# Performance work log

Measured on AMD Instinct MI355X. Metric: run time of the kernel, lower is better.

The kernel has to match this reference:

```python
import math
import jax, jax.numpy as jnp
import numpy as np

CANTOR_DEPTH = 8
CANTOR_TEMPERATURE = 1.0
SEQ_LEN = 4096


def _cantor_positions(depth_max):
    positions = [np.array([0.0, 1.0])]
    for _ in range(1, depth_max):
        prev = positions[-1]
        new = []
        for i in range(len(prev) - 1):
            left = prev[i]
            right = prev[i + 1]
            third = (right - left) / 3.0
            new.append(left)
            new.append(left + third)
        new.append(prev[-1])
        positions.append(np.array(new))
    return positions


def _cantor_indices(seq_len, depth_max):
    # indices[d] = unique sorted long indices of Cantor positions at depth d
    pos = _cantor_positions(depth_max)
    out = []
    for d in range(depth_max):
        idx = np.unique((pos[d] * (seq_len - 1)).astype(np.int64))
        out.append(jnp.asarray(idx))
    return out


# number of depths actually used in the forward loop
_N_DEPTHS = min(CANTOR_DEPTH, int(math.log2(SEQ_LEN)) + 2)
# get_cantor_indices caps depth at cantor_depth - 1 implicitly via list length
CANTOR_IDX = _cantor_indices(SEQ_LEN, CANTOR_DEPTH)


def setup_inputs() -> dict:
    key0 = jax.random.key(0)
    ks = jax.random.split(key0, 4)
    B, S, D = 8, SEQ_LEN, 512
    return {
        "query": jax.random.normal(ks[0], (B, S, D), dtype=jnp.float32),
        "key": jax.random.normal(ks[1], (B, S, D), dtype=jnp.float32),
        "value": jax.random.normal(ks[2], (B, S, D), dtype=jnp.float32),
        "t": jax.random.normal(ks[3], (B,), dtype=jnp.float32),
        "scale_weights": jnp.ones((CANTOR_DEPTH,), dtype=jnp.float32),
        "scale_temperature": jnp.ones((1,), dtype=jnp.float32),
    }


def reference(query, key, value, t, scale_weights, scale_temperature):
    D = key.shape[-1]
    inv_scale = 1.0 / (math.sqrt(D) * CANTOR_TEMPERATURE)
    scale_outputs = []
    for depth in range(_N_DEPTHS):
        idx = CANTOR_IDX[depth]            # static, <= 2^depth + 1 indices
        sk = key[:, idx]                   # [B, Nd, D] gather
        sv = value[:, idx]                 # [B, Nd, D]
        scores = jnp.einsum("bqd,bkd->bqk", query, sk) * inv_scale
        attn = jax.nn.softmax(scores, axis=-1)
        scale_outputs.append(jnp.einsum("bqk,bkd->bqd", attn, sv))
    stacked = jnp.stack(scale_outputs, axis=0)  # [depths, B, Q, D]
    w = jax.nn.softmax(scale_weights[: len(scale_outputs)] / scale_temperature[0])
    out = jnp.sum(stacked * w[:, None, None, None], axis=0)  # [B, Q, D]
    # torch .squeeze(1) is a no-op here since Q != 1
    return out
```

## Files before the change

### kernel.cpp

```cpp
#include <hip/hip_runtime.h>

#define NDEPTH 8
#define NK 129
#define SEQB 4096
#define DIM 512

typedef short bf16x8 __attribute__((ext_vector_type(8)));
typedef float f32x4  __attribute__((ext_vector_type(4)));

struct CTab { int uidx[NK]; int minD[NK]; int count; };

static constexpr CTab make_ctab() {
    CTab T{};
    double pos[NDEPTH][NK] = {}; int cnt[NDEPTH] = {};
    pos[0][0] = 0.0; pos[0][1] = 1.0; cnt[0] = 2;
    for (int d = 1; d < NDEPTH; ++d) {
        const int n = cnt[d - 1]; int m = 0;
        for (int i = 0; i < n - 1; ++i) {
            const double left = pos[d - 1][i], right = pos[d - 1][i + 1];
            const double third = (right - left) / 3.0;
            pos[d][m++] = left; pos[d][m++] = left + third;
        }
        pos[d][m++] = pos[d - 1][n - 1]; cnt[d] = m;
    }
    int idx[NDEPTH][NK] = {}; int icnt[NDEPTH] = {};
    for (int d = 0; d < NDEPTH; ++d) {
        int m = 0;
        for (int i = 0; i < cnt[d]; ++i) {
            const long long v = (long long)(pos[d][i] * 4095.0);
            bool dup = false;
            for (int k = 0; k < m; ++k) if (idx[d][k] == (int)v) dup = true;
            if (!dup) idx[d][m++] = (int)v;
        }
        icnt[d] = m;
    }
    int u[2 * NK] = {}; int un = 0;
    for (int d = 0; d < NDEPTH; ++d)
        for (int i = 0; i < icnt[d]; ++i) {
            const int v = idx[d][i]; bool f = false;
            for (int k = 0; k < un; ++k) if (u[k] == v) f = true;
            if (!f && un < 2 * NK) u[un++] = v;
        }
    for (int i = 1; i < un; ++i) {
        const int key = u[i]; int k = i - 1;
        while (k >= 0 && u[k] > key) { u[k + 1] = u[k]; --k; }
        u[k + 1] = key;
    }
    T.count = un;
    for (int i = 0; i < un && i < NK; ++i) {
        T.uidx[i] = u[i];
        int md = NDEPTH;
        for (int d = 0; d < NDEPTH && md == NDEPTH; ++d)
            for (int k = 0; k < icnt[d]; ++k)
                if (idx[d][k] == u[i]) { md = d; break; }
        T.minD[i] = md;
    }
    return T;
}
static constexpr CTab h_ct = make_ctab();
static_assert(h_ct.count == NK, "cantor union size mismatch");
__device__ __constant__ CTab g_ct = h_ct;

__device__ __forceinline__ short f2bf(float f) {
    union { float f; unsigned u; } v; v.f = f;
    unsigned r = v.u + 0x7fffu + ((v.u >> 16) & 1u);
    return (short)(r >> 16);
}

#define WSK_ELEMS (8 * 144 * 512)

__global__ __launch_bounds__(256) void ufa_prep(
    const float* __restrict__ K, const float* __restrict__ V,
    short* __restrict__ ws)
{
    short* wsK  = ws;
    short* wsVt = ws + WSK_ELEMS;
    if (blockIdx.x < 1152) {
        const int b = blockIdx.x / 144, key = blockIdx.x % 144;
        short* dst = wsK + ((size_t)b * 144 + key) * 512;
        if (key < NK) {
            const float* src = K + ((size_t)b * SEQB + g_ct.uidx[key]) * DIM;
            for (int i = threadIdx.x; i < 512; i += 256) dst[i] = f2bf(src[i]);
        } else {
            for (int i = threadIdx.x; i < 512; i += 256) dst[i] = 0;
        }
    } else {
        __shared__ float tr[16][132];
        const int id = blockIdx.x - 1152;
        const int b = id >> 5, dc = id & 31;
        const float* Vb = V + (size_t)b * SEQB * DIM + dc * 16;
        const int kk = (int)threadIdx.x >> 4, d = (int)threadIdx.x & 15;
        #pragma unroll
        for (int it = 0; it < 9; ++it) {
            const int k = it * 16 + kk;
            if (k < NK) tr[d][k] = Vb[(size_t)g_ct.uidx[k] * DIM + d];
        }
        __syncthreads();
        short* dst = wsVt + ((size_t)b * 512 + dc * 16) * 192;
        for (int idx = threadIdx.x; idx < 16 * 192; idx += 256) {
            const int dd = idx / 192, k = idx - dd * 192;
            dst[idx] = (k < NK) ? f2bf(tr[dd][k]) : (short)0;
        }
    }
}

__global__ __launch_bounds__(64, 4) void ufa_main(
    const float* __restrict__ Q, const short* __restrict__ ws,
    const float* __restrict__ SW, const float* __restrict__ ST,
    float* __restrict__ Out)
{
    __shared__ short c_lds[16 * 200];

    const short* wsK  = ws;
    const short* wsVt = ws + WSK_ELEMS;

    const int lane = (int)threadIdx.x;
    const int m    = lane & 15;
    const int quad = lane >> 4;
    const int b    = (int)blockIdx.x >> 8;
    const int q0   = ((int)blockIdx.x & 255) << 4;

    float wgt[NDEPTH];
    {
        const float it = 1.0f / ST[0];
        float mx = -3.0e38f;
        #pragma unroll
        for (int d = 0; d < NDEPTH; ++d) { wgt[d] = SW[d] * it; mx = fmaxf(mx, wgt[d]); }
        float sum = 0.0f;
        #pragma unroll
        for (int d = 0; d < NDEPTH; ++d) { wgt[d] = __expf(wgt[d] - mx); sum += wgt[d]; }
        const float is = 1.0f / sum;
        #pragma unroll
        for (int d = 0; d < NDEPTH; ++d) wgt[d] *= is;
    }

    f32x4 acc[9];
    #pragma unroll
    for (int tt = 0; tt < 9; ++tt) acc[tt] = (f32x4){0.f, 0.f, 0.f, 0.f};

    const float* Qb = Q + ((size_t)b * SEQB + q0 + m) * DIM;
    const short* Kb = wsK + (size_t)b * 144 * 512;

    #pragma unroll
    for (int c = 0; c < 8; ++c) {
        bf16x8 aq[2];
        #pragma unroll
        for (int ks = 0; ks < 2; ++ks) {
            const float* qp = Qb + c * 64 + ks * 32 + quad * 8;
            const float4 x = *(const float4*)qp;
            const float4 y = *(const float4*)(qp + 4);
            aq[ks][0] = f2bf(x.x); aq[ks][1] = f2bf(x.y);
            aq[ks][2] = f2bf(x.z); aq[ks][3] = f2bf(x.w);
            aq[ks][4] = f2bf(y.x); aq[ks][5] = f2bf(y.y);
            aq[ks][6] = f2bf(y.z); aq[ks][7] = f2bf(y.w);
        }
        #pragma unroll
        for (int ks = 0; ks < 2; ++ks) {
            #pragma unroll
            for (int tt = 0; tt < 9; ++tt) {
                const bf16x8 bk = *(const bf16x8*)&Kb[(size_t)(tt * 16 + m) * 512
                                                     + c * 64 + ks * 32 + quad * 8];
                acc[tt] = __builtin_amdgcn_mfma_f32_16x16x32_bf16(aq[ks], bk, acc[tt], 0, 0, 0);
            }
        }
    }

    const float inv_scale = 0.04419417382415922f;
    int md9[9];
    #pragma unroll
    for (int tt = 0; tt < 9; ++tt) {
        const int j = tt * 16 + m;
        md9[tt] = (j < NK) ? g_ct.minD[j] : NDEPTH;
    }
    float ev[9][4], mxr[4];
    #pragma unroll
    for (int i = 0; i < 4; ++i) mxr[i] = -3.0e38f;
    #pragma unroll
    for (int tt = 0; tt < 9; ++tt) {
        const bool valid = (tt * 16 + m) < NK;
        #pragma unroll
        for (int i = 0; i < 4; ++i) {
            const float s = valid ? acc[tt][i] * inv_scale : -3.0e38f;
            ev[tt][i] = s;
            mxr[i] = fmaxf(mxr[i], s);
        }
    }
    #pragma unroll
    for (int off = 1; off < 16; off <<= 1)
        #pragma unroll
        for (int i = 0; i < 4; ++i) mxr[i] = fmaxf(mxr[i], __shfl_xor(mxr[i], off));

    float P[4][NDEPTH];
    #pragma unroll
    for (int i = 0; i < 4; ++i)
        #pragma unroll
        for (int d = 0; d < NDEPTH; ++d) P[i][d] = 0.0f;
    #pragma unroll
    for (int tt = 0; tt < 9; ++tt) {
        const int md = md9[tt];
        #pragma unroll
        for (int i = 0; i < 4; ++i) {
            const float e = __expf(ev[tt][i] - mxr[i]);
            ev[tt][i] = e;
            #pragma unroll
            for (int d = 0; d < NDEPTH; ++d) P[i][d] += (md == d) ? e : 0.0f;
        }
    }
    #pragma unroll
    for (int off = 1; off < 16; off <<= 1)
        #pragma unroll
        for (int i = 0; i < 4; ++i)
            #pragma unroll
            for (int d = 0; d < NDEPTH; ++d) P[i][d] += __shfl_xor(P[i][d], off);

    float T[4][NDEPTH];
    #pragma unroll
    for (int i = 0; i < 4; ++i) {
        float L = 0.0f, Lc[NDEPTH];
        #pragma unroll
        for (int d = 0; d < NDEPTH; ++d) { L += P[i][d]; Lc[d] = L; }
        float ta = 0.0f;
        #pragma unroll
        for (int d = NDEPTH - 1; d >= 0; --d) { ta += wgt[d] / Lc[d]; T[i][d] = ta; }
    }
    #pragma unroll
    for (int tt = 0; tt < 10; ++tt) {
        const int j = tt * 16 + m;
        #pragma unroll
        for (int i = 0; i < 4; ++i) {
            float cv = 0.0f;
            if (tt < 9 && j < NK) {
                const int md = md9[tt];
                float tv = 0.0f;
                #pragma unroll
                for (int d = 0; d < NDEPTH; ++d) tv = (md == d) ? T[i][d] : tv;
                cv = ev[tt][i] * tv;
            }
            c_lds[(quad * 4 + i) * 200 + j] = f2bf(cv);
        }
    }
    __syncthreads();

    bf16x8 ac[5];
    #pragma unroll
    for (int ks = 0; ks < 5; ++ks)
        ac[ks] = *(const bf16x8*)&c_lds[m * 200 + ks * 32 + quad * 8];

    const short* Vtb = wsVt + (size_t)b * 512 * 192;
    float* Ob = Out + ((size_t)b * SEQB + q0) * DIM;

    #pragma unroll
    for (int c2 = 0; c2 < 8; ++c2) {
        #pragma unroll
        for (int nt = 0; nt < 4; ++nt) {
            f32x4 o = (f32x4){0.f, 0.f, 0.f, 0.f};
            #pragma unroll
            for (int ks = 0; ks < 5; ++ks) {
                const bf16x8 bv = *(const bf16x8*)&Vtb[(size_t)(c2 * 64 + nt * 16 + m) * 192
                                                       + ks * 32 + quad * 8];
                o = __builtin_amdgcn_mfma_f32_16x16x32_bf16(ac[ks], bv, o, 0, 0, 0);
            }
            const int n0 = c2 * 64 + nt * 16;
            #pragma unroll
            for (int i = 0; i < 4; ++i)
                Ob[(size_t)(quad * 4 + i) * DIM + n0 + m] = o[i];
        }
    }
}

extern "C" void kernel_launch(void* const* d_in, const int* in_sizes, int n_in,
                              void* d_out, int out_size, void* d_ws, size_t ws_size,
                              hipStream_t stream) {
    const float* Q  = (const float*)d_in[0];
    const float* K  = (const float*)d_in[1];
    const float* V  = (const float*)d_in[2];
    const float* SW = (const float*)d_in[4];
    const float* ST = (const float*)d_in[5];
    float* Out = (float*)d_out;
    short* ws  = (short*)d_ws;

    ufa_prep<<<dim3(1152 + 256), dim3(256), 0, stream>>>(K, V, ws);
    ufa_main<<<dim3(2048), dim3(64), 0, stream>>>(Q, ws, SW, ST, Out);
}
```

Before: 257.1 us.

## Split main attention kernel across four waves per block

The main kernel goes from one wave per block to four. Each wave computes a partial Q·K^T over a quarter of the head dimension, and the partials are summed through shared memory. The multi-scale softmax is then spread across the waves by query row, and each wave computes a quarter of the output columns in the P·V product. The aim is more concurrent work per block to hide memory latency, in exchange for extra shared-memory reductions and barriers.

```diff
diff --git a/kernel.cpp b/kernel.cpp
--- a/kernel.cpp
+++ b/kernel.cpp
@@ -104,17 +104,23 @@
     }
 }
 
-__global__ __launch_bounds__(64, 4) void ufa_main(
+#define SSTR 148
+#define CSTR 168
+
+__global__ __launch_bounds__(256, 6) void ufa_main(
     const float* __restrict__ Q, const short* __restrict__ ws,
     const float* __restrict__ SW, const float* __restrict__ ST,
     float* __restrict__ Out)
 {
-    __shared__ short c_lds[16 * 200];
+    __shared__ float sbuf[2][16][SSTR];
+    __shared__ short c_lds[16][CSTR];
 
     const short* wsK  = ws;
     const short* wsVt = ws + WSK_ELEMS;
 
-    const int lane = (int)threadIdx.x;
+    const int t    = (int)threadIdx.x;
+    const int w    = t >> 6;
+    const int lane = t & 63;
     const int m    = lane & 15;
     const int quad = lane >> 4;
     const int b    = (int)blockIdx.x >> 8;
@@ -138,133 +144,122 @@
     #pragma unroll
     for (int tt = 0; tt < 9; ++tt) acc[tt] = (f32x4){0.f, 0.f, 0.f, 0.f};
 
-    const float* Qb = Q + ((size_t)b * SEQB + q0 + m) * DIM;
-    const short* Kb = wsK + (size_t)b * 144 * 512;
-
-    #pragma unroll
-    for (int c = 0; c < 8; ++c) {
-        bf16x8 aq[2];
-        #pragma unroll
-        for (int ks = 0; ks < 2; ++ks) {
-            const float* qp = Qb + c * 64 + ks * 32 + quad * 8;
-            const float4 x = *(const float4*)qp;
-            const float4 y = *(const float4*)(qp + 4);
-            aq[ks][0] = f2bf(x.x); aq[ks][1] = f2bf(x.y);
-            aq[ks][2] = f2bf(x.z); aq[ks][3] = f2bf(x.w);
-            aq[ks][4] = f2bf(y.x); aq[ks][5] = f2bf(y.y);
-            aq[ks][6] = f2bf(y.z); aq[ks][7] = f2bf(y.w);
-        }
-        #pragma unroll
-        for (int ks = 0; ks < 2; ++ks) {
-            #pragma unroll
-            for (int tt = 0; tt < 9; ++tt) {
-                const bf16x8 bk = *(const bf16x8*)&Kb[(size_t)(tt * 16 + m) * 512
-                                                     + c * 64 + ks * 32 + quad * 8];
-                acc[tt] = __builtin_amdgcn_mfma_f32_16x16x32_bf16(aq[ks], bk, acc[tt], 0, 0, 0);
-            }
-        }
-    }
-
-    const float inv_scale = 0.04419417382415922f;
-    int md9[9];
-    #pragma unroll
-    for (int tt = 0; tt < 9; ++tt) {
-        const int j = tt * 16 + m;
-        md9[tt] = (j < NK) ? g_ct.minD[j] : NDEPTH;
-    }
-    float ev[9][4], mxr[4];
-    #pragma unroll
-    for (int i = 0; i < 4; ++i) mxr[i] = -3.0e38f;
-    #pragma unroll
-    for (int tt = 0; tt < 9; ++tt) {
-        const bool valid = (tt * 16 + m) < NK;
-        #pragma unroll
-        for (int i = 0; i < 4; ++i) {
-            const float s = valid ? acc[tt][i] * inv_scale : -3.0e38f;
-            ev[tt][i] = s;
-            mxr[i] = fmaxf(mxr[i], s);
-        }
-    }
-    #pragma unroll
-    for (int off = 1; off < 16; off <<= 1)
-        #pragma unroll
-        for (int i = 0; i < 4; ++i) mxr[i] = fmaxf(mxr[i], __shfl_xor(mxr[i], off));
-
-    float P[4][NDEPTH];
-    #pragma unroll
-    for (int i = 0; i < 4; ++i)
-        #pragma unroll
-        for (int d = 0; d < NDEPTH; ++d) P[i][d] = 0.0f;
-    #pragma unroll
-    for (int tt = 0; tt < 9; ++tt) {
-        const int md = md9[tt];
-        #pragma unroll
-        for (int i = 0; i < 4; ++i) {
-            const float e = __expf(ev[tt][i] - mxr[i]);
-            ev[tt][i] = e;
-            #pragma unroll
-            for (int d = 0; d < NDEPTH; ++d) P[i][d] += (md == d) ? e : 0.0f;
-        }
-    }
-    #pragma unroll
-    for (int off = 1; off < 16; off <<= 1)
-        #pragma unroll
-        for (int i = 0; i < 4; ++i)
-            #pragma unroll
-            for (int d = 0; d < NDEPTH; ++d) P[i][d] += __shfl_xor(P[i][d], off);
-
-    float T[4][NDEPTH];
-    #pragma unroll
-    for (int i = 0; i < 4; ++i) {
-        float L = 0.0f, Lc[NDEPTH];
-        #pragma unroll
-        for (int d = 0; d < NDEPTH; ++d) { L += P[i][d]; Lc[d] = L; }
-        float ta = 0.0f;
-        #pragma unroll
-        for (int d = NDEPTH - 1; d >= 0; --d) { ta += wgt[d] / Lc[d]; T[i][d] = ta; }
-    }
-    #pragma unroll
-    for (int tt = 0; tt < 10; ++tt) {
-        const int j = tt * 16 + m;
-        #pragma unroll
-        for (int i = 0; i < 4; ++i) {
-            float cv = 0.0f;
-            if (tt < 9 && j < NK) {
-                const int md = md9[tt];
-                float tv = 0.0f;
-                #pragma unroll
-                for (int d = 0; d < NDEPTH; ++d) tv = (md == d) ? T[i][d] : tv;
-                cv = ev[tt][i] * tv;
-            }
-            c_lds[(quad * 4 + i) * 200 + j] = f2bf(cv);
-        }
-    }
-    __syncthreads();
-
-    bf16x8 ac[5];
-    #pragma unroll
-    for (int ks = 0; ks < 5; ++ks)
-        ac[ks] = *(const bf16x8*)&c_lds[m * 200 + ks * 32 + quad * 8];
-
-    const short* Vtb = wsVt + (size_t)b * 512 * 192;
-    float* Ob = Out + ((size_t)b * SEQB + q0) * DIM;
-
-    #pragma unroll
-    for (int c2 = 0; c2 < 8; ++c2) {
-        #pragma unroll
-        for (int nt = 0; nt < 4; ++nt) {
-            f32x4 o = (f32x4){0.f, 0.f, 0.f, 0.f};
-            #pragma unroll
-            for (int ks = 0; ks < 5; ++ks) {
-                const bf16x8 bv = *(const bf16x8*)&Vtb[(size_t)(c2 * 64 + nt * 16 + m) * 192
-                                                       + ks * 32 + quad * 8];
-                o = __builtin_amdgcn_mfma_f32_16x16x32_bf16(ac[ks], bv, o, 0, 0, 0);
-            }
-            const int n0 = c2 * 64 + nt * 16;
+    const float* Qb = Q + ((size_t)b * SEQB + q0 + m) * DIM + w * 128;
+    const short* Kb = wsK + (size_t)b * 144 * 512 + w * 128;
+
+    #pragma unroll
+    for (int ks = 0; ks < 4; ++ks) {
+        const float* qp = Qb + ks * 32 + quad * 8;
+        const float4 x = *(const float4*)qp;
+        const float4 y = *(const float4*)(qp + 4);
+        bf16x8 aq;
+        aq[0] = f2bf(x.x); aq[1] = f2bf(x.y); aq[2] = f2bf(x.z); aq[3] = f2bf(x.w);
+        aq[4] = f2bf(y.x); aq[5] = f2bf(y.y); aq[6] = f2bf(y.z); aq[7] = f2bf(y.w);
+        #pragma unroll
+        for (int tt = 0; tt < 9; ++tt) {
+            const bf16x8 bk = *(const bf16x8*)&Kb[(size_t)(tt * 16 + m) * 512
+                                                 + ks * 32 + quad * 8];
+            acc[tt] = __builtin_amdgcn_mfma_f32_16x16x32_bf16(aq, bk, acc[tt], 0, 0, 0);
+        }
+    }
+
+    if (w & 1) {
+        float* Bf = &sbuf[w >> 1][0][0];
+        #pragma unroll
+        for (int tt = 0; tt < 9; ++tt)
             #pragma unroll
             for (int i = 0; i < 4; ++i)
-                Ob[(size_t)(quad * 4 + i) * DIM + n0 + m] = o[i];
-        }
+                Bf[(quad * 4 + i) * SSTR + tt * 16 + m] = acc[tt][i];
+    }
+    __syncthreads();
+    if (!(w & 1)) {
+        float* Bf = &sbuf[w >> 1][0][0];
+        #pragma unroll
+        for (int tt = 0; tt < 9; ++tt)
+            #pragma unroll
+            for (int i = 0; i < 4; ++i) {
+                const int a = (quad * 4 + i) * SSTR + tt * 16 + m;
+                Bf[a] += acc[tt][i];
+            }
+    }
+    __syncthreads();
+
+    const float inv_scale = 0.04419417382415922f;
+    const int k0 = lane, k1 = 64 + lane, k2 = 128 + lane;
+    const int  md0 = g_ct.minD[k0];
+    const int  md1 = g_ct.minD[k1];
+    const bool v2  = (k2 < NK);
+    float cr0[4], cr1[4], cr2[4];
+
+    #pragma unroll
+    for (int rr = 0; rr < 4; ++rr) {
+        const int r = w * 4 + rr;
+        const float S0 = (sbuf[0][r][k0] + sbuf[1][r][k0]) * inv_scale;
+        const float S1 = (sbuf[0][r][k1] + sbuf[1][r][k1]) * inv_scale;
+        const float S2 = v2 ? (sbuf[0][r][128] + sbuf[1][r][128]) * inv_scale : -3.0e38f;
+        float mx = fmaxf(fmaxf(S0, S1), S2);
+        #pragma unroll
+        for (int off = 1; off < 64; off <<= 1) mx = fmaxf(mx, __shfl_xor(mx, off));
+
+        const float e0 = __expf(S0 - mx);
+        const float e1 = __expf(S1 - mx);
+        const float e2 = v2 ? __expf(S2 - mx) : 0.0f;
+
+        float P[NDEPTH];
+        #pragma unroll
+        for (int d = 0; d < NDEPTH; ++d)
+            P[d] = ((md0 == d) ? e0 : 0.0f) + ((md1 == d) ? e1 : 0.0f)
+                 + ((v2 && md0 == md0 && g_ct.minD[128] == d) ? e2 : 0.0f);
+        #pragma unroll
+        for (int off = 1; off < 64; off <<= 1)
+            #pragma unroll
+            for (int d = 0; d < NDEPTH; ++d) P[d] += __shfl_xor(P[d], off);
+
+        float L = 0.0f, Tv[NDEPTH];
+        #pragma unroll
+        for (int d = 0; d < NDEPTH; ++d) { L += P[d]; Tv[d] = L; }
+        float ta = 0.0f;
+        #pragma unroll
+        for (int d = NDEPTH - 1; d >= 0; --d) { ta += wgt[d] / Tv[d]; Tv[d] = ta; }
+
+        float tv0 = 0.0f, tv1 = 0.0f, tv2 = 0.0f;
+        #pragma unroll
+        for (int d = 0; d < NDEPTH; ++d) {
+            tv0 = (md0 == d) ? Tv[d] : tv0;
+            tv1 = (md1 == d) ? Tv[d] : tv1;
+            tv2 = (v2 && g_ct.minD[128] == d) ? Tv[d] : tv2;
+        }
+        cr0[rr] = e0 * tv0; cr1[rr] = e1 * tv1; cr2[rr] = e2 * tv2;
+    }
+    #pragma unroll
+    for (int rr = 0; rr < 4; ++rr) {
+        const int r = w * 4 + rr;
+        c_lds[r][k0] = f2bf(cr0[rr]);
+        c_lds[r][k1] = f2bf(cr1[rr]);
+        if (lane < 32) c_lds[r][128 + lane] = (lane == 0) ? f2bf(cr2[rr]) : (short)0;
+    }
+    __syncthreads();
+
+    bf16x8 ac[5];
+    #pragma unroll
+    for (int ks = 0; ks < 5; ++ks)
+        ac[ks] = *(const bf16x8*)&c_lds[m][ks * 32 + quad * 8];
+
+    const short* Vtb = wsVt + (size_t)b * 512 * 192 + (size_t)w * 128 * 192;
+    float* Ob = Out + ((size_t)b * SEQB + q0) * DIM + w * 128;
+
+    #pragma unroll
+    for (int nt = 0; nt < 8; ++nt) {
+        f32x4 o = (f32x4){0.f, 0.f, 0.f, 0.f};
+        #pragma unroll
+        for (int ks = 0; ks < 5; ++ks) {
+            const bf16x8 bv = *(const bf16x8*)&Vtb[(size_t)(nt * 16 + m) * 192
+                                                   + ks * 32 + quad * 8];
+            o = __builtin_amdgcn_mfma_f32_16x16x32_bf16(ac[ks], bv, o, 0, 0, 0);
+        }
+        #pragma unroll
+        for (int i = 0; i < 4; ++i)
+            Ob[(size_t)(quad * 4 + i) * DIM + nt * 16 + m] = o[i];
     }
 }
 
@@ -280,5 +275,5 @@
     short* ws  = (short*)d_ws;
 
     ufa_prep<<<dim3(1152 + 256), dim3(256), 0, stream>>>(K, V, ws);
-    ufa_main<<<dim3(2048), dim3(64), 0, stream>>>(Q, ws, SW, ST, Out);
-}
+    ufa_main<<<dim3(2048), dim3(256), 0, stream>>>(Q, ws, SW, ST, Out);
+}
```

Result: slower. 272.9 us (+6.1%).

## Stage K and V tiles in shared LDS with double-buffering across 4-wave blocks

Applied to the files above, without the earlier changes.

The main kernel moves from one wave per block to four waves per block, with the four waves covering 64 query rows. The gathered K and transposed V are now staged cooperatively into double-buffered LDS, with register prefetch of the next chunk, instead of each wave reading them from global memory. Q is converted to bf16 once up front, and the V workspace row pitch shrinks from 192 to 160. This cuts redundant global/L2 traffic for K and V, at the cost of more LDS, more registers and block-wide barriers, plus fewer blocks (512) to fill the GPU.

```diff
diff --git a/kernel.cpp b/kernel.cpp
--- a/kernel.cpp
+++ b/kernel.cpp
@@ -96,29 +96,39 @@
             if (k < NK) tr[d][k] = Vb[(size_t)g_ct.uidx[k] * DIM + d];
         }
         __syncthreads();
-        short* dst = wsVt + ((size_t)b * 512 + dc * 16) * 192;
-        for (int idx = threadIdx.x; idx < 16 * 192; idx += 256) {
-            const int dd = idx / 192, k = idx - dd * 192;
+        short* dst = wsVt + ((size_t)b * 512 + dc * 16) * 160;
+        for (int idx = threadIdx.x; idx < 16 * 160; idx += 256) {
+            const int dd = idx / 160, k = idx - dd * 160;
             dst[idx] = (k < NK) ? f2bf(tr[dd][k]) : (short)0;
         }
     }
 }
 
-__global__ __launch_bounds__(64, 4) void ufa_main(
+#define KCH 20736
+#define VCH 21504
+#define V0_OFF 43008
+#define SMEM_BYTES 64512
+
+__global__ __launch_bounds__(256, 2) void ufa_main(
     const float* __restrict__ Q, const short* __restrict__ ws,
     const float* __restrict__ SW, const float* __restrict__ ST,
     float* __restrict__ Out)
 {
-    __shared__ short c_lds[16 * 200];
+    __shared__ char smem[SMEM_BYTES];
 
     const short* wsK  = ws;
     const short* wsVt = ws + WSK_ELEMS;
 
-    const int lane = (int)threadIdx.x;
+    const int t    = (int)threadIdx.x;
+    const int w    = t >> 6;
+    const int lane = t & 63;
     const int m    = lane & 15;
     const int quad = lane >> 4;
-    const int b    = (int)blockIdx.x >> 8;
-    const int q0   = ((int)blockIdx.x & 255) << 4;
+    const int b    = (int)blockIdx.x >> 6;
+    const int q0w  = (((int)blockIdx.x & 63) << 6) + w * 16;
+
+    const short* wsKb  = wsK  + (size_t)b * 144 * 512;
+    const short* wsVtb = wsVt + (size_t)b * 512 * 160;
 
     float wgt[NDEPTH];
     {
@@ -134,35 +144,73 @@
         for (int d = 0; d < NDEPTH; ++d) wgt[d] *= is;
     }
 
+    bf16x8 sreg[5];
+    #define K_LOAD(c)                                                        \
+        _Pragma("unroll")                                                    \
+        for (int j = 0; j < 5; ++j) {                                        \
+            const int i = t + j * 256;                                       \
+            if (i < 1152) {                                                  \
+                const int r = i >> 3, p = i & 7;                             \
+                sreg[j] = *(const bf16x8*)(wsKb + (size_t)r * 512 + (c) * 64 + p * 8); \
+            }                                                                \
+        }
+    #define K_WRITE(c)                                                       \
+        {   char* dbuf = smem + ((c) & 1) * KCH;                             \
+            _Pragma("unroll")                                                \
+            for (int j = 0; j < 5; ++j) {                                    \
+                const int i = t + j * 256;                                   \
+                if (i < 1152) {                                              \
+                    const int r = i >> 3, p = i & 7;                         \
+                    *(bf16x8*)(dbuf + r * 144 + p * 16) = sreg[j];           \
+                }                                                            \
+            }                                                                \
+        }
+
+    K_LOAD(0);
+
+    bf16x8 qf[16];
+    const float* Qb = Q + ((size_t)b * SEQB + q0w + m) * DIM;
+    #pragma unroll
+    for (int ks = 0; ks < 16; ++ks) {
+        const float* qp = Qb + ks * 32 + quad * 8;
+        const float4 x = *(const float4*)qp;
+        const float4 y = *(const float4*)(qp + 4);
+        qf[ks][0] = f2bf(x.x); qf[ks][1] = f2bf(x.y);
+        qf[ks][2] = f2bf(x.z); qf[ks][3] = f2bf(x.w);
+        qf[ks][4] = f2bf(y.x); qf[ks][5] = f2bf(y.y);
+        qf[ks][6] = f2bf(y.z); qf[ks][7] = f2bf(y.w);
+    }
+
+    K_WRITE(0);
+    __syncthreads();
+
     f32x4 acc[9];
     #pragma unroll
     for (int tt = 0; tt < 9; ++tt) acc[tt] = (f32x4){0.f, 0.f, 0.f, 0.f};
 
-    const float* Qb = Q + ((size_t)b * SEQB + q0 + m) * DIM;
-    const short* Kb = wsK + (size_t)b * 144 * 512;
-
-    #pragma unroll
     for (int c = 0; c < 8; ++c) {
-        bf16x8 aq[2];
-        #pragma unroll
-        for (int ks = 0; ks < 2; ++ks) {
-            const float* qp = Qb + c * 64 + ks * 32 + quad * 8;
-            const float4 x = *(const float4*)qp;
-            const float4 y = *(const float4*)(qp + 4);
-            aq[ks][0] = f2bf(x.x); aq[ks][1] = f2bf(x.y);
-            aq[ks][2] = f2bf(x.z); aq[ks][3] = f2bf(x.w);
-            aq[ks][4] = f2bf(y.x); aq[ks][5] = f2bf(y.y);
-            aq[ks][6] = f2bf(y.z); aq[ks][7] = f2bf(y.w);
-        }
-        #pragma unroll
-        for (int ks = 0; ks < 2; ++ks) {
+        if (c < 7) { K_LOAD(c + 1); }
+        const char* buf = smem + (c & 1) * KCH;
+        #pragma unroll
+        for (int kk = 0; kk < 2; ++kk) {
             #pragma unroll
             for (int tt = 0; tt < 9; ++tt) {
-                const bf16x8 bk = *(const bf16x8*)&Kb[(size_t)(tt * 16 + m) * 512
-                                                     + c * 64 + ks * 32 + quad * 8];
-                acc[tt] = __builtin_amdgcn_mfma_f32_16x16x32_bf16(aq[ks], bk, acc[tt], 0, 0, 0);
-            }
-        }
+                const bf16x8 bk = *(const bf16x8*)(buf + (tt * 16 + m) * 144
+                                                   + (kk * 4 + quad) * 16);
+                acc[tt] = __builtin_amdgcn_mfma_f32_16x16x32_bf16(
+                              qf[c * 2 + kk], bk, acc[tt], 0, 0, 0);
+            }
+        }
+        if (c < 7) { K_WRITE(c + 1); }
+        __syncthreads();
+    }
+
+    bf16x8 vreg[5];
+    #pragma unroll
+    for (int j = 0; j < 5; ++j) {
+        const int i = t + j * 256;
+        const int r = i / 20, p = i - r * 20;
+        vreg[j] = *(const bf16x8*)(wsVtb + (size_t)r * 160 + p * 8);
     }
 
     const float inv_scale = 0.04419417382415922f;
@@ -223,6 +271,8 @@
         #pragma unroll
         for (int d = NDEPTH - 1; d >= 0; --d) { ta += wgt[d] / Lc[d]; T[i][d] = ta; }
     }
+
+    short* c_lds = (short*)(smem) + w * (16 * 168);
     #pragma unroll
     for (int tt = 0; tt < 10; ++tt) {
         const int j = tt * 16 + m;
@@ -236,28 +286,42 @@
                 for (int d = 0; d < NDEPTH; ++d) tv = (md == d) ? T[i][d] : tv;
                 cv = ev[tt][i] * tv;
             }
-            c_lds[(quad * 4 + i) * 200 + j] = f2bf(cv);
-        }
+            c_lds[(quad * 4 + i) * 168 + j] = f2bf(cv);
+        }
+    }
+    bf16x8 ac[5];
+    #pragma unroll
+    for (int ks = 0; ks < 5; ++ks)
+        ac[ks] = *(const bf16x8*)&c_lds[m * 168 + ks * 32 + quad * 8];
+
+    #pragma unroll
+    for (int j = 0; j < 5; ++j) {
+        const int i = t + j * 256;
+        const int r = i / 20, p = i - r * 20;
+        *(bf16x8*)(smem + V0_OFF + r * 336 + p * 16) = vreg[j];
     }
     __syncthreads();
 
-    bf16x8 ac[5];
-    #pragma unroll
-    for (int ks = 0; ks < 5; ++ks)
-        ac[ks] = *(const bf16x8*)&c_lds[m * 200 + ks * 32 + quad * 8];
-
-    const short* Vtb = wsVt + (size_t)b * 512 * 192;
-    float* Ob = Out + ((size_t)b * SEQB + q0) * DIM;
-
-    #pragma unroll
+    float* Ob = Out + ((size_t)b * SEQB + q0w) * DIM;
+
     for (int c2 = 0; c2 < 8; ++c2) {
+        if (c2 < 7) {
+            #pragma unroll
+            for (int j = 0; j < 5; ++j) {
+                const int i = t + j * 256;
+                const int r = i / 20, p = i - r * 20;
+                vreg[j] = *(const bf16x8*)(wsVtb + (size_t)(c2 + 1) * 64 * 160
+                                           + (size_t)r * 160 + p * 8);
+            }
+        }
+        const char* buf = smem + ((c2 & 1) ? 0 : V0_OFF);
         #pragma unroll
         for (int nt = 0; nt < 4; ++nt) {
             f32x4 o = (f32x4){0.f, 0.f, 0.f, 0.f};
             #pragma unroll
             for (int ks = 0; ks < 5; ++ks) {
-                const bf16x8 bv = *(const bf16x8*)&Vtb[(size_t)(c2 * 64 + nt * 16 + m) * 192
-                                                       + ks * 32 + quad * 8];
+                const bf16x8 bv = *(const bf16x8*)(buf + (nt * 16 + m) * 336
+                                                   + (ks * 4 + quad) * 16);
                 o = __builtin_amdgcn_mfma_f32_16x16x32_bf16(ac[ks], bv, o, 0, 0, 0);
             }
             const int n0 = c2 * 64 + nt * 16;
@@ -265,6 +329,16 @@
             for (int i = 0; i < 4; ++i)
                 Ob[(size_t)(quad * 4 + i) * DIM + n0 + m] = o[i];
         }
+        if (c2 < 7) {
+            char* dbuf = smem + ((c2 & 1) ? V0_OFF : 0);
+            #pragma unroll
+            for (int j = 0; j < 5; ++j) {
+                const int i = t + j * 256;
+                const int r = i / 20, p = i - r * 20;
+                *(bf16x8*)(dbuf + r * 336 + p * 16) = vreg[j];
+            }
+        }
+        __syncthreads();
     }
 }
 
@@ -280,5 +354,5 @@
     short* ws  = (short*)d_ws;
 
     ufa_prep<<<dim3(1152 + 256), dim3(256), 0, stream>>>(K, V, ws);
-    ufa_main<<<dim3(2048), dim3(64), 0, stream>>>(Q, ws, SW, ST, Out);
-}
+    ufa_main<<<dim3(512), dim3(256), 0, stream>>>(Q, ws, SW, ST, Out);
+}
```

After: 213.3 us. -17.0%, faster.

## Stage K/V tiles in LDS with double buffering across four-wave blocks

Applied to the files above, without the earlier changes.

Restructures the main kernel into 256-thread blocks of four waves that share K and V^T chunks. The chunks are staged into swizzled LDS with direct global-to-LDS loads and double buffering, replacing per-wave global reads. Keys are reordered by minimum depth so per-depth softmax sums can use static ranges. MFMA operands are swapped so each lane writes a contiguous float4 of output, and the whole Q row is converted to bf16 up front. This adds register pressure (16 Q fragments) and block-level barriers in exchange for shared K/V reuse.

```diff
diff --git a/kernel.cpp b/kernel.cpp
--- a/kernel.cpp
+++ b/kernel.cpp
@@ -6,9 +6,15 @@
 #define DIM 512
 
 typedef short bf16x8 __attribute__((ext_vector_type(8)));
+typedef short bf16x4 __attribute__((ext_vector_type(4)));
 typedef float f32x4  __attribute__((ext_vector_type(4)));
 
-struct CTab { int uidx[NK]; int minD[NK]; int count; };
+struct CTab {
+    int uidx[NK]; int minD[NK];
+    int sidx[NK];
+    int SB[NDEPTH + 1];
+    int count;
+};
 
 static constexpr CTab make_ctab() {
     CTab T{};
@@ -55,16 +61,36 @@
                 if (idx[d][k] == u[i]) { md = d; break; }
         T.minD[i] = md;
     }
+    int n = 0;
+    for (int d = 0; d < NDEPTH; ++d) {
+        T.SB[d] = n;
+        for (int i = 0; i < un && i < NK; ++i)
+            if (T.minD[i] == d) T.sidx[n++] = T.uidx[i];
+    }
+    T.SB[NDEPTH] = n;
     return T;
 }
 static constexpr CTab h_ct = make_ctab();
 static_assert(h_ct.count == NK, "cantor union size mismatch");
+static_assert(h_ct.SB[NDEPTH] == NK, "sorted union size mismatch");
 __device__ __constant__ CTab g_ct = h_ct;
+
+__host__ __device__ constexpr int depth_of(int key) {
+    int d = NDEPTH - 1;
+    for (int x = NDEPTH - 1; x >= 0; --x) if (key < h_ct.SB[x + 1]) d = x;
+    return d;
+}
 
 __device__ __forceinline__ short f2bf(float f) {
     union { float f; unsigned u; } v; v.f = f;
     unsigned r = v.u + 0x7fffu + ((v.u >> 16) & 1u);
     return (short)(r >> 16);
+}
+
+__device__ __forceinline__ void gl_lds16(const void* g, void* lds) {
+    __builtin_amdgcn_global_load_lds(
+        (const __attribute__((address_space(1))) unsigned int*)g,
+        (__attribute__((address_space(3))) unsigned int*)lds, 16, 0, 0);
 }
 
 #define WSK_ELEMS (8 * 144 * 512)
@@ -79,7 +105,7 @@
         const int b = blockIdx.x / 144, key = blockIdx.x % 144;
         short* dst = wsK + ((size_t)b * 144 + key) * 512;
         if (key < NK) {
-            const float* src = K + ((size_t)b * SEQB + g_ct.uidx[key]) * DIM;
+            const float* src = K + ((size_t)b * SEQB + g_ct.sidx[key]) * DIM;
             for (int i = threadIdx.x; i < 512; i += 256) dst[i] = f2bf(src[i]);
         } else {
             for (int i = threadIdx.x; i < 512; i += 256) dst[i] = 0;
@@ -93,7 +119,7 @@
         #pragma unroll
         for (int it = 0; it < 9; ++it) {
             const int k = it * 16 + kk;
-            if (k < NK) tr[d][k] = Vb[(size_t)g_ct.uidx[k] * DIM + d];
+            if (k < NK) tr[d][k] = Vb[(size_t)g_ct.sidx[k] * DIM + d];
         }
         __syncthreads();
         short* dst = wsVt + ((size_t)b * 512 + dc * 16) * 192;
@@ -104,21 +130,32 @@
     }
 }
 
-__global__ __launch_bounds__(64, 4) void ufa_main(
+#define KCH 18432
+#define VCH 24576
+#define CLDS_OFF 36864
+#define CSTR 200
+#define SMEM_BYTES 62976
+
+__global__ __launch_bounds__(256, 2) void ufa_main(
     const float* __restrict__ Q, const short* __restrict__ ws,
     const float* __restrict__ SW, const float* __restrict__ ST,
     float* __restrict__ Out)
 {
-    __shared__ short c_lds[16 * 200];
+    __shared__ char smem[SMEM_BYTES];
 
     const short* wsK  = ws;
     const short* wsVt = ws + WSK_ELEMS;
 
-    const int lane = (int)threadIdx.x;
+    const int t    = (int)threadIdx.x;
+    const int w    = t >> 6;
+    const int lane = t & 63;
     const int m    = lane & 15;
     const int quad = lane >> 4;
-    const int b    = (int)blockIdx.x >> 8;
-    const int q0   = ((int)blockIdx.x & 255) << 4;
+    const int b    = (int)blockIdx.x >> 6;
+    const int q0w  = (((int)blockIdx.x & 63) << 6) + w * 16;
+
+    const short* wsKb  = wsK  + (size_t)b * 144 * 512;
+    const short* wsVb  = wsVt + (size_t)b * 512 * 192;
 
     float wgt[NDEPTH];
     {
@@ -134,137 +171,175 @@
         for (int d = 0; d < NDEPTH; ++d) wgt[d] *= is;
     }
 
+    #define STAGE_K(c, dst)                                                  \
+        for (int g = w; g < 18; g += 4) {                                    \
+            const int off  = g * 1024 + lane * 16;                           \
+            const int row  = off >> 7;                                       \
+            const int slot = (off >> 4) & 7;                                 \
+            const int slog = slot ^ (row & 7);                               \
+            gl_lds16(wsKb + (size_t)row * 512 + (c) * 64 + slog * 8,         \
+                     (dst) + g * 1024);                                      \
+        }
+    #define STAGE_V(c2, dst)                                                 \
+        for (int g = w; g < 24; g += 4) {                                    \
+            const int off  = g * 1024 + lane * 16;                           \
+            const int row  = off / 384;                                      \
+            const int rem  = off - row * 384;                                \
+            const int slot = rem >> 4;                                       \
+            const int slog = (slot & ~7) | ((slot & 7) ^ (row & 7));         \
+            gl_lds16(wsVb + (size_t)((c2) * 64 + row) * 192 + slog * 8,      \
+                     (dst) + g * 1024);                                      \
+        }
+
+    char* const kbuf0 = smem;
+    char* const kbuf1 = smem + KCH;
+
+    STAGE_K(0, kbuf0);
+
+    bf16x8 qf[16];
+    const float* Qb = Q + ((size_t)b * SEQB + q0w + m) * DIM;
+    #pragma unroll
+    for (int ks = 0; ks < 16; ++ks) {
+        const float* qp = Qb + ks * 32 + quad * 8;
+        const float4 x = *(const float4*)qp;
+        const float4 y = *(const float4*)(qp + 4);
+        qf[ks][0] = f2bf(x.x); qf[ks][1] = f2bf(x.y);
+        qf[ks][2] = f2bf(x.z); qf[ks][3] = f2bf(x.w);
+        qf[ks][4] = f2bf(y.x); qf[ks][5] = f2bf(y.y);
+        qf[ks][6] = f2bf(y.z); qf[ks][7] = f2bf(y.w);
+    }
+    __syncthreads();
+
     f32x4 acc[9];
     #pragma unroll
     for (int tt = 0; tt < 9; ++tt) acc[tt] = (f32x4){0.f, 0.f, 0.f, 0.f};
 
-    const float* Qb = Q + ((size_t)b * SEQB + q0 + m) * DIM;
-    const short* Kb = wsK + (size_t)b * 144 * 512;
-
-    #pragma unroll
     for (int c = 0; c < 8; ++c) {
-        bf16x8 aq[2];
-        #pragma unroll
-        for (int ks = 0; ks < 2; ++ks) {
-            const float* qp = Qb + c * 64 + ks * 32 + quad * 8;
-            const float4 x = *(const float4*)qp;
-            const float4 y = *(const float4*)(qp + 4);
-            aq[ks][0] = f2bf(x.x); aq[ks][1] = f2bf(x.y);
-            aq[ks][2] = f2bf(x.z); aq[ks][3] = f2bf(x.w);
-            aq[ks][4] = f2bf(y.x); aq[ks][5] = f2bf(y.y);
-            aq[ks][6] = f2bf(y.z); aq[ks][7] = f2bf(y.w);
-        }
-        #pragma unroll
-        for (int ks = 0; ks < 2; ++ks) {
+        if (c < 7) { STAGE_K(c + 1, (c & 1) ? kbuf0 : kbuf1); }
+        const char* buf = (c & 1) ? kbuf1 : kbuf0;
+        #pragma unroll
+        for (int kk = 0; kk < 2; ++kk) {
             #pragma unroll
             for (int tt = 0; tt < 9; ++tt) {
-                const bf16x8 bk = *(const bf16x8*)&Kb[(size_t)(tt * 16 + m) * 512
-                                                     + c * 64 + ks * 32 + quad * 8];
-                acc[tt] = __builtin_amdgcn_mfma_f32_16x16x32_bf16(aq[ks], bk, acc[tt], 0, 0, 0);
+                const int row  = tt * 16 + m;
+                const int slog = (kk * 4 + quad) ^ (row & 7);
+                const bf16x8 bk = *(const bf16x8*)(buf + row * 128 + slog * 16);
+                acc[tt] = __builtin_amdgcn_mfma_f32_16x16x32_bf16(
+                              bk, qf[c * 2 + kk], acc[tt], 0, 0, 0);
             }
         }
-    }
+        __syncthreads();
+    }
+
+    STAGE_V(0, smem);
 
     const float inv_scale = 0.04419417382415922f;
-    int md9[9];
+    float ev[9][4];
+    float mx = -3.0e38f;
     #pragma unroll
     for (int tt = 0; tt < 9; ++tt) {
-        const int j = tt * 16 + m;
-        md9[tt] = (j < NK) ? g_ct.minD[j] : NDEPTH;
-    }
-    float ev[9][4], mxr[4];
-    #pragma unroll
-    for (int i = 0; i < 4; ++i) mxr[i] = -3.0e38f;
+        #pragma unroll
+        for (int i = 0; i < 4; ++i) {
+            float s = acc[tt][i] * inv_scale;
+            if (tt == 8) s = (quad == 0 && i == 0) ? s : -3.0e38f;
+            ev[tt][i] = s;
+            mx = fmaxf(mx, s);
+        }
+    }
+    mx = fmaxf(mx, __shfl_xor(mx, 16));
+    mx = fmaxf(mx, __shfl_xor(mx, 32));
+
+    float P[NDEPTH];
+    #pragma unroll
+    for (int d = 0; d < NDEPTH; ++d) P[d] = 0.0f;
     #pragma unroll
     for (int tt = 0; tt < 9; ++tt) {
-        const bool valid = (tt * 16 + m) < NK;
+        const int dLo = depth_of(tt * 16);
+        const int dHi = depth_of(tt * 16 + 15 < NK ? tt * 16 + 15 : NK - 1);
         #pragma unroll
         for (int i = 0; i < 4; ++i) {
-            const float s = valid ? acc[tt][i] * inv_scale : -3.0e38f;
-            ev[tt][i] = s;
-            mxr[i] = fmaxf(mxr[i], s);
-        }
-    }
-    #pragma unroll
-    for (int off = 1; off < 16; off <<= 1)
-        #pragma unroll
-        for (int i = 0; i < 4; ++i) mxr[i] = fmaxf(mxr[i], __shfl_xor(mxr[i], off));
-
-    float P[4][NDEPTH];
-    #pragma unroll
-    for (int i = 0; i < 4; ++i)
-        #pragma unroll
-        for (int d = 0; d < NDEPTH; ++d) P[i][d] = 0.0f;
+            const float e = __expf(ev[tt][i] - mx);
+            ev[tt][i] = e;
+            if (dLo == dHi) {
+                P[dLo] += e;
+            } else {
+                const int key = tt * 16 + quad * 4 + i;
+                #pragma unroll
+                for (int d = dLo; d <= dHi; ++d) {
+                    const bool in = (key >= h_ct.SB[d]) && (key < h_ct.SB[d + 1]);
+                    P[d] += in ? e : 0.0f;
+                }
+            }
+        }
+    }
+    #pragma unroll
+    for (int d = 0; d < NDEPTH; ++d) {
+        P[d] += __shfl_xor(P[d], 16);
+        P[d] += __shfl_xor(P[d], 32);
+    }
+
+    float Lc = 0.0f, Tsf[NDEPTH];
+    #pragma unroll
+    for (int d = 0; d < NDEPTH; ++d) { Lc += P[d]; Tsf[d] = Lc; }
+    {
+        float ta = 0.0f;
+        #pragma unroll
+        for (int d = NDEPTH - 1; d >= 0; --d) { ta += wgt[d] / Tsf[d]; Tsf[d] = ta; }
+    }
+
+    short* crow = (short*)(smem + CLDS_OFF) + (w * 16 + m) * CSTR;
     #pragma unroll
     for (int tt = 0; tt < 9; ++tt) {
-        const int md = md9[tt];
+        const int dLo = depth_of(tt * 16);
+        const int dHi = depth_of(tt * 16 + 15 < NK ? tt * 16 + 15 : NK - 1);
+        bf16x4 pk;
         #pragma unroll
         for (int i = 0; i < 4; ++i) {
-            const float e = __expf(ev[tt][i] - mxr[i]);
-            ev[tt][i] = e;
-            #pragma unroll
-            for (int d = 0; d < NDEPTH; ++d) P[i][d] += (md == d) ? e : 0.0f;
-        }
-    }
-    #pragma unroll
-    for (int off = 1; off < 16; off <<= 1)
-        #pragma unroll
-        for (int i = 0; i < 4; ++i)
-            #pragma unroll
-            for (int d = 0; d < NDEPTH; ++d) P[i][d] += __shfl_xor(P[i][d], off);
-
-    float T[4][NDEPTH];
-    #pragma unroll
-    for (int i = 0; i < 4; ++i) {
-        float L = 0.0f, Lc[NDEPTH];
-        #pragma unroll
-        for (int d = 0; d < NDEPTH; ++d) { L += P[i][d]; Lc[d] = L; }
-        float ta = 0.0f;
-        #pragma unroll
-        for (int d = NDEPTH - 1; d >= 0; --d) { ta += wgt[d] / Lc[d]; T[i][d] = ta; }
-    }
-    #pragma unroll
-    for (int tt = 0; tt < 10; ++tt) {
-        const int j = tt * 16 + m;
-        #pragma unroll
-        for (int i = 0; i < 4; ++i) {
-            float cv = 0.0f;
-            if (tt < 9 && j < NK) {
-                const int md = md9[tt];
-                float tv = 0.0f;
+            float tv = Tsf[dLo];
+            if (dLo != dHi) {
+                const int key = tt * 16 + quad * 4 + i;
                 #pragma unroll
-                for (int d = 0; d < NDEPTH; ++d) tv = (md == d) ? T[i][d] : tv;
-                cv = ev[tt][i] * tv;
+                for (int d = dLo + 1; d <= dHi; ++d)
+                    tv = (key >= h_ct.SB[d]) ? Tsf[d] : tv;
             }
-            c_lds[(quad * 4 + i) * 200 + j] = f2bf(cv);
-        }
-    }
+            pk[i] = f2bf(ev[tt][i] * tv);
+        }
+        *(bf16x4*)(crow + tt * 16 + quad * 4) = pk;
+    }
+    *(bf16x4*)(crow + 144 + quad * 4) = (bf16x4){0, 0, 0, 0};
+
     __syncthreads();
 
     bf16x8 ac[5];
-    #pragma unroll
-    for (int ks = 0; ks < 5; ++ks)
-        ac[ks] = *(const bf16x8*)&c_lds[m * 200 + ks * 32 + quad * 8];
-
-    const short* Vtb = wsVt + (size_t)b * 512 * 192;
-    float* Ob = Out + ((size_t)b * SEQB + q0) * DIM;
-
-    #pragma unroll
+    {
+        const short* cr = (const short*)(smem + CLDS_OFF) + (w * 16 + m) * CSTR;
+        #pragma unroll
+        for (int ks = 0; ks < 5; ++ks)
+            ac[ks] = *(const bf16x8*)(cr + ks * 32 + quad * 8);
+    }
+    __syncthreads();
+
+    char* const vbuf0 = smem;
+    char* const vbuf1 = smem + VCH;
+    float* Obm = Out + ((size_t)b * SEQB + q0w + m) * DIM + quad * 4;
+
     for (int c2 = 0; c2 < 8; ++c2) {
+        if (c2 < 7) { STAGE_V(c2 + 1, (c2 & 1) ? vbuf0 : vbuf1); }
+        const char* buf = (c2 & 1) ? vbuf1 : vbuf0;
         #pragma unroll
         for (int nt = 0; nt < 4; ++nt) {
             f32x4 o = (f32x4){0.f, 0.f, 0.f, 0.f};
             #pragma unroll
             for (int ks = 0; ks < 5; ++ks) {
-                const bf16x8 bv = *(const bf16x8*)&Vtb[(size_t)(c2 * 64 + nt * 16 + m) * 192
-                                                       + ks * 32 + quad * 8];
-                o = __builtin_amdgcn_mfma_f32_16x16x32_bf16(ac[ks], bv, o, 0, 0, 0);
+                const int row  = nt * 16 + m;
+                const int slot = ks * 4 + quad;
+                const int slog = (slot & ~7) | ((slot & 7) ^ (row & 7));
+                const bf16x8 bv = *(const bf16x8*)(buf + row * 384 + slog * 16);
+                o = __builtin_amdgcn_mfma_f32_16x16x32_bf16(bv, ac[ks], o, 0, 0, 0);
             }
-            const int n0 = c2 * 64 + nt * 16;
-            #pragma unroll
-            for (int i = 0; i < 4; ++i)
-                Ob[(size_t)(quad * 4 + i) * DIM + n0 + m] = o[i];
-        }
+            *(f32x4*)(Obm + c2 * 64 + nt * 16) = o;
+        }
+        if (c2 < 7) __syncthreads();
     }
 }
 
@@ -280,5 +355,5 @@
     short* ws  = (short*)d_ws;
 
     ufa_prep<<<dim3(1152 + 256), dim3(256), 0, stream>>>(K, V, ws);
-    ufa_main<<<dim3(2048), dim3(64), 0, stream>>>(Q, ws, SW, ST, Out);
-}
+    ufa_main<<<dim3(512), dim3(256), 0, stream>>>(Q, ws, SW, ST, Out);
+}
```

Result: faster. 207.5 us (-19.3%).
